# Kernel tuning notes

Measured on AMD Instinct MI355X. Metric: run time of the kernel, lower is better.

Reference implementation:

```python
import jax, jax.numpy as jnp
import numpy as np

N_ATOMS = 3
HIDDEN = 256
N_PAIRS = N_ATOMS * (N_ATOMS - 1) // 2  # 3
BATCH = 500000


def setup_inputs() -> dict:
    key = jax.random.key(0)
    ks = jax.random.split(key, 8)
    s1 = 1.0 / np.sqrt(N_PAIRS)
    s2 = 1.0 / np.sqrt(HIDDEN)
    return {
        "x": jax.random.normal(ks[0], (BATCH, N_ATOMS * 3), dtype=jnp.float32),
        "W1": jax.random.normal(ks[1], (N_PAIRS, HIDDEN), dtype=jnp.float32) * s1,
        "b1": jnp.zeros((HIDDEN,), dtype=jnp.float32),
        "W2": jax.random.normal(ks[2], (HIDDEN, HIDDEN), dtype=jnp.float32) * s2,
        "b2": jnp.zeros((HIDDEN,), dtype=jnp.float32),
        "W3": jax.random.normal(ks[3], (HIDDEN, 3), dtype=jnp.float32) * s2,
        "b3": jnp.zeros((3,), dtype=jnp.float32),
    }


def reference(x, W1, b1, W2, b2, W3, b3):
    # --- pairwise bond lengths (vectorized over batch) ---
    pts = x.reshape(-1, N_ATOMS, 3)                       # [B, n_atoms, 3]
    iu, ju = np.triu_indices(N_ATOMS, 1)                  # static index arrays
    diff = pts[:, iu, :] - pts[:, ju, :]                  # [B, n_pairs, 3]
    r = jnp.sqrt(jnp.sum(diff * diff, axis=-1))           # [B, n_pairs]
    # --- MLP: Dense->relu->Dense->relu->Dense (sizes=[256,256,3]) ---
    h = jax.nn.relu(r @ W1 + b1)                          # [B, 256]
    h = jax.nn.relu(h @ W2 + b2)                          # [B, 256]
    w = h @ W3 + b3                                       # [B, 3] -> (w00, w11, w01)
    # --- analytic eigenvalues of symmetric 2x2 [[w00,w01],[w01,w11]] ---
    # eigh returns ascending order: mean -/+ radius
    m = 0.5 * (w[:, 0] + w[:, 1])
    d = 0.5 * (w[:, 0] - w[:, 1])
    rad = jnp.sqrt(d * d + w[:, 2] * w[:, 2])
    return jnp.stack([m - rad, m + rad], axis=-1)         # [B, 2]
```

## Files before the change

kernel.cpp:

```cpp
#include <hip/hip_runtime.h>
#include <hip/hip_bf16.h>
#include <stdint.h>

typedef __attribute__((ext_vector_type(8))) short short8;
typedef __attribute__((ext_vector_type(4))) float f32x4;

#define NCHUNK 15625
#define NBLK 256
#define NTHR 512
#define NWAVE_TOT (NBLK * 8)

#define FRAG_OFF   0
#define W1_OFF     131072
#define B2_OFF     135168
#define SCR_OFF    136192
#define LDS_TOTAL  152576

__device__ __forceinline__ uint32_t cvtpk(float lo, float hi) {
    uint32_t r;
    asm("v_cvt_pk_bf16_f32 %0, %1, %2" : "=v"(r) : "v"(lo), "v"(hi));
    return r;
}

__device__ __forceinline__ int sig2(int mp) {
    int t = mp >> 4, gm = (mp >> 2) & 3, r = mp & 3;
    return ((t >> 1) << 5) + (gm << 3) + ((t & 1) << 2) + r;
}

__global__ __launch_bounds__(NTHR, 2) void fused_kernel(
    const float* __restrict__ x,  const float* __restrict__ W1,
    const float* __restrict__ b1, const float* __restrict__ W2,
    const float* __restrict__ b2, const float* __restrict__ W3,
    const float* __restrict__ b3, float* __restrict__ out)
{
    extern __shared__ char smem[];
    uint4*  frag4 = (uint4*)(smem + FRAG_OFF);
    float4* w1lds = (float4*)(smem + W1_OFF);
    float4* b2lds = (float4*)(smem + B2_OFF);
    float*  scrf  = (float*)(smem + SCR_OFF);
    uint4*  scr4  = (uint4*)(smem + SCR_OFF);

    const int tid  = threadIdx.x;
    const int lane = tid & 63;
    const int g    = lane >> 4;
    const int lr   = lane & 15;

    if (tid < 256)
        w1lds[tid] = make_float4(W1[tid], W1[256 + tid], W1[512 + tid], b1[tid]);
    else if (tid < 320)
        b2lds[tid - 256] = ((const float4*)b2)[tid - 256];

    const uint4* gw2 = (const uint4*)W2;
    for (int p = 0; p < 16; ++p) {
        __syncthreads();
        scr4[tid]       = gw2[p * 1024 + tid];
        scr4[tid + 512] = gw2[p * 1024 + 512 + tid];
        __syncthreads();
        int t   = tid >> 5;
        int l   = (tid & 31) + ((p & 1) << 5);
        int c16 = l & 15;
        int s   = p >> 1;
        int c   = sig2(t * 16 + c16);
        int rowbase = ((l >> 4) & 1) * 8;
        float f[8];
#pragma unroll
        for (int j = 0; j < 8; ++j) f[j] = scrf[(rowbase + j) * 256 + c];
        uint4 wv;
        wv.x = cvtpk(f[0], f[1]); wv.y = cvtpk(f[2], f[3]);
        wv.z = cvtpk(f[4], f[5]); wv.w = cvtpk(f[6], f[7]);
        frag4[(s * 16 + t) * 64 + l] = wv;
    }
    __syncthreads();

    short8 w3f[8];
#pragma unroll
    for (int s2 = 0; s2 < 8; ++s2) {
        float f3[8];
#pragma unroll
        for (int j = 0; j < 8; ++j) {
            int kk = s2 * 32 + g * 8 + j;
            f3[j] = (lr < 3) ? W3[kk * 3 + lr] : 0.0f;
        }
        union { short8 s8; uint32_t u[4]; } pw;
        pw.u[0] = cvtpk(f3[0], f3[1]); pw.u[1] = cvtpk(f3[2], f3[3]);
        pw.u[2] = cvtpk(f3[4], f3[5]); pw.u[3] = cvtpk(f3[6], f3[7]);
        w3f[s2] = pw.s8;
    }
    const float b30 = b3[0], b31 = b3[1], b32 = b3[2];

    const short8* afr = (const short8*)(smem + FRAG_OFF);
    const int gwave = blockIdx.x * 8 + (tid >> 6);

    for (int chunk = gwave; chunk < NCHUNK; chunk += NWAVE_TOT) {
        const int row0 = chunk * 32;

        float q0[2], q1[2], q2[2];
#pragma unroll
        for (int nt = 0; nt < 2; ++nt) {
            const float* xp = x + (size_t)(row0 + nt * 16 + lr) * 9;
            float a0 = xp[0], a1 = xp[1], a2 = xp[2], a3 = xp[3], a4 = xp[4];
            float a5 = xp[5], a6 = xp[6], a7 = xp[7], a8 = xp[8];
            float d0 = a0 - a3, d1 = a1 - a4, d2 = a2 - a5;
            float e0 = a0 - a6, e1 = a1 - a7, e2 = a2 - a8;
            float f0 = a3 - a6, f1 = a4 - a7, f2 = a5 - a8;
            q0[nt] = sqrtf(fmaf(d0, d0, fmaf(d1, d1, d2 * d2)));
            q1[nt] = sqrtf(fmaf(e0, e0, fmaf(e1, e1, e2 * e2)));
            q2[nt] = sqrtf(fmaf(f0, f0, fmaf(f1, f1, f2 * f2)));
        }

        f32x4 acc[16][2];
#pragma unroll
        for (int t = 0; t < 16; ++t) {
            int bc4 = (((t >> 1) << 5) + (g << 3) + ((t & 1) << 2)) >> 2;
            float4 bv = b2lds[bc4];
            f32x4 bi; bi[0] = bv.x; bi[1] = bv.y; bi[2] = bv.z; bi[3] = bv.w;
            acc[t][0] = bi; acc[t][1] = bi;
        }

#pragma unroll 1
        for (int s = 0; s < 8; ++s) {
            float4 wv[8];
#pragma unroll
            for (int j = 0; j < 8; ++j) wv[j] = w1lds[s * 32 + g * 8 + j];
            short8 hb[2];
#pragma unroll
            for (int nt = 0; nt < 2; ++nt) {
                union { short8 s8; uint32_t u[4]; } pk;
#pragma unroll
                for (int jj = 0; jj < 4; ++jj) {
                    float4 wa = wv[2 * jj], wb = wv[2 * jj + 1];
                    float ha = fmaf(q0[nt], wa.x, fmaf(q1[nt], wa.y, fmaf(q2[nt], wa.z, wa.w)));
                    float hc = fmaf(q0[nt], wb.x, fmaf(q1[nt], wb.y, fmaf(q2[nt], wb.z, wb.w)));
                    pk.u[jj] = cvtpk(fmaxf(ha, 0.f), fmaxf(hc, 0.f));
                }
                hb[nt] = pk.s8;
            }
#pragma unroll
            for (int t = 0; t < 16; ++t) {
                short8 av = afr[(s * 16 + t) * 64 + lane];
                acc[t][0] = __builtin_amdgcn_mfma_f32_16x16x32_bf16(av, hb[0], acc[t][0], 0, 0, 0);
                acc[t][1] = __builtin_amdgcn_mfma_f32_16x16x32_bf16(av, hb[1], acc[t][1], 0, 0, 0);
            }
        }

#pragma unroll
        for (int nt = 0; nt < 2; ++nt) {
            f32x4 D = {0.f, 0.f, 0.f, 0.f};
#pragma unroll
            for (int s2 = 0; s2 < 8; ++s2) {
                union { short8 s8; uint32_t u[4]; } pb;
                pb.u[0] = cvtpk(fmaxf(acc[2 * s2][nt][0], 0.f), fmaxf(acc[2 * s2][nt][1], 0.f));
                pb.u[1] = cvtpk(fmaxf(acc[2 * s2][nt][2], 0.f), fmaxf(acc[2 * s2][nt][3], 0.f));
                pb.u[2] = cvtpk(fmaxf(acc[2 * s2 + 1][nt][0], 0.f), fmaxf(acc[2 * s2 + 1][nt][1], 0.f));
                pb.u[3] = cvtpk(fmaxf(acc[2 * s2 + 1][nt][2], 0.f), fmaxf(acc[2 * s2 + 1][nt][3], 0.f));
                D = __builtin_amdgcn_mfma_f32_16x16x32_bf16(w3f[s2], pb.s8, D, 0, 0, 0);
            }
            if (g == 0) {
                float w0 = D[0] + b30, w1v = D[1] + b31, wc = D[2] + b32;
                float mm = 0.5f * (w0 + w1v), dd = 0.5f * (w0 - w1v);
                float rad = sqrtf(fmaf(dd, dd, wc * wc));
                int row = row0 + nt * 16 + lr;
                *(float2*)(out + (size_t)row * 2) = make_float2(mm - rad, mm + rad);
            }
        }
    }
}

extern "C" void kernel_launch(void* const* d_in, const int* in_sizes, int n_in,
                              void* d_out, int out_size, void* d_ws, size_t ws_size,
                              hipStream_t stream) {
    const float* x  = (const float*)d_in[0];
    const float* W1 = (const float*)d_in[1];
    const float* b1 = (const float*)d_in[2];
    const float* W2 = (const float*)d_in[3];
    const float* b2 = (const float*)d_in[4];
    const float* W3 = (const float*)d_in[5];
    const float* b3 = (const float*)d_in[6];
    float* out = (float*)d_out;

    (void)d_ws; (void)ws_size;

    (void)hipFuncSetAttribute((const void*)fused_kernel,
                              hipFuncAttributeMaxDynamicSharedMemorySize, LDS_TOTAL);

    fused_kernel<<<NBLK, NTHR, LDS_TOTAL, stream>>>(x, W1, b1, W2, b2, W3, b3, out);
}
```

Baseline: 159.1 us.

## Switch to 32x32x16 MFMA, compute layer 1 and bias via MFMA, prefetch x

Replaces the 16x16x32 MFMA tiling with 32x32x16 bf16 MFMAs, so each wave handles one 32-row chunk with 8 accumulator tiles. Layer 1 (bond lengths times W1 plus b1) and the b2 bias initialisation now run as MFMAs against padded fragments in LDS, replacing the VALU FMA loops. W2 fragments are repacked with a swizzled column layout to match. The next chunk's x rows are prefetched into registers to hide global load latency. This reduces VALU work and load stalls, at the cost of extra wasted MFMA work on zero-padded operands and higher register pressure.

```diff
diff --git a/kernel.cpp b/kernel.cpp
--- a/kernel.cpp
+++ b/kernel.cpp
@@ -2,29 +2,27 @@
 #include <hip/hip_bf16.h>
 #include <stdint.h>
 
-typedef __attribute__((ext_vector_type(8))) short short8;
-typedef __attribute__((ext_vector_type(4))) float f32x4;
+typedef __attribute__((ext_vector_type(8)))  short short8;
+typedef __attribute__((ext_vector_type(16))) float f32x16;
 
 #define NCHUNK 15625
 #define NBLK 256
 #define NTHR 512
 #define NWAVE_TOT (NBLK * 8)
 
-#define FRAG_OFF   0
-#define W1_OFF     131072
-#define B2_OFF     135168
-#define SCR_OFF    136192
-#define LDS_TOTAL  152576
+#define SW(v) ((((v) & ~12u)) | (((v) & 4u) << 1) | (((v) & 8u) >> 1))
+
+#define A2_OFF   0
+#define A1_OFF   131072
+#define Z_OFF    135168
+#define A3_OFF   135184
+#define SCR_OFF  136720
+#define LDS_TOTAL 153104
 
 __device__ __forceinline__ uint32_t cvtpk(float lo, float hi) {
     uint32_t r;
     asm("v_cvt_pk_bf16_f32 %0, %1, %2" : "=v"(r) : "v"(lo), "v"(hi));
     return r;
-}
-
-__device__ __forceinline__ int sig2(int mp) {
-    int t = mp >> 4, gm = (mp >> 2) & 3, r = mp & 3;
-    return ((t >> 1) << 5) + (gm << 3) + ((t & 1) << 2) + r;
 }
 
 __global__ __launch_bounds__(NTHR, 2) void fused_kernel(
@@ -34,135 +32,153 @@
     const float* __restrict__ b3, float* __restrict__ out)
 {
     extern __shared__ char smem[];
-    uint4*  frag4 = (uint4*)(smem + FRAG_OFF);
-    float4* w1lds = (float4*)(smem + W1_OFF);
-    float4* b2lds = (float4*)(smem + B2_OFF);
-    float*  scrf  = (float*)(smem + SCR_OFF);
-    uint4*  scr4  = (uint4*)(smem + SCR_OFF);
-
-    const int tid  = threadIdx.x;
-    const int lane = tid & 63;
-    const int g    = lane >> 4;
-    const int lr   = lane & 15;
-
-    if (tid < 256)
-        w1lds[tid] = make_float4(W1[tid], W1[256 + tid], W1[512 + tid], b1[tid]);
-    else if (tid < 320)
-        b2lds[tid - 256] = ((const float4*)b2)[tid - 256];
-
+    uint4* frag4 = (uint4*)(smem + A2_OFF);
+    float* scrf  = (float*)(smem + SCR_OFF);
+    uint4* scr4  = (uint4*)(smem + SCR_OFF);
+
+    const int tid = threadIdx.x;
+    const int l   = tid & 63;
+    const int hi  = l >> 5;
+    const int c   = l & 31;
+
+    {
+        int fr = tid >> 6, l2 = tid & 63;
+        if (l2 < 32) {
+            int row = fr * 32 + l2;
+            uint4 v;
+            v.x = cvtpk(W1[row], W1[256 + row]);
+            v.y = cvtpk(W1[512 + row], b1[row]);
+            v.z = 0; v.w = 0;
+            ((uint4*)(smem + A1_OFF))[fr * 32 + l2] = v;
+        }
+        if (tid == 511) ((uint4*)(smem + Z_OFF))[0] = make_uint4(0, 0, 0, 0);
+        if (tid < 96) {
+            int fr3 = tid / 6, rem = tid % 6, hi2 = rem / 3, c2 = rem % 3;
+            int kb = 16 * fr3 + 8 * hi2;
+            uint4 v;
+            v.x = cvtpk(W3[(kb + 0) * 3 + c2], W3[(kb + 1) * 3 + c2]);
+            v.y = cvtpk(W3[(kb + 2) * 3 + c2], W3[(kb + 3) * 3 + c2]);
+            v.z = cvtpk(W3[(kb + 4) * 3 + c2], W3[(kb + 5) * 3 + c2]);
+            v.w = cvtpk(W3[(kb + 6) * 3 + c2], W3[(kb + 7) * 3 + c2]);
+            ((uint4*)(smem + A3_OFF))[fr3 * 6 + rem] = v;
+        }
+    }
     const uint4* gw2 = (const uint4*)W2;
-    for (int p = 0; p < 16; ++p) {
+    for (int kt = 0; kt < 16; ++kt) {
         __syncthreads();
-        scr4[tid]       = gw2[p * 1024 + tid];
-        scr4[tid + 512] = gw2[p * 1024 + 512 + tid];
+        scr4[tid]       = gw2[kt * 1024 + tid];
+        scr4[tid + 512] = gw2[kt * 1024 + 512 + tid];
         __syncthreads();
-        int t   = tid >> 5;
-        int l   = (tid & 31) + ((p & 1) << 5);
-        int c16 = l & 15;
-        int s   = p >> 1;
-        int c   = sig2(t * 16 + c16);
-        int rowbase = ((l >> 4) & 1) * 8;
+        int mt = tid >> 6, l2 = tid & 63, hi2 = l2 >> 5, c2 = l2 & 31;
+        int col = 32 * mt + (int)SW((unsigned)c2);
         float f[8];
 #pragma unroll
-        for (int j = 0; j < 8; ++j) f[j] = scrf[(rowbase + j) * 256 + c];
-        uint4 wv;
-        wv.x = cvtpk(f[0], f[1]); wv.y = cvtpk(f[2], f[3]);
-        wv.z = cvtpk(f[4], f[5]); wv.w = cvtpk(f[6], f[7]);
-        frag4[(s * 16 + t) * 64 + l] = wv;
+        for (int j = 0; j < 8; ++j) {
+            int lrow = 8 * (j >> 2) + 4 * hi2 + (j & 3);
+            f[j] = scrf[lrow * 256 + col];
+        }
+        uint4 v;
+        v.x = cvtpk(f[0], f[1]); v.y = cvtpk(f[2], f[3]);
+        v.z = cvtpk(f[4], f[5]); v.w = cvtpk(f[6], f[7]);
+        frag4[(kt * 8 + mt) * 64 + l2] = v;
     }
     __syncthreads();
 
-    short8 w3f[8];
-#pragma unroll
-    for (int s2 = 0; s2 < 8; ++s2) {
-        float f3[8];
-#pragma unroll
-        for (int j = 0; j < 8; ++j) {
-            int kk = s2 * 32 + g * 8 + j;
-            f3[j] = (lr < 3) ? W3[kk * 3 + lr] : 0.0f;
-        }
-        union { short8 s8; uint32_t u[4]; } pw;
-        pw.u[0] = cvtpk(f3[0], f3[1]); pw.u[1] = cvtpk(f3[2], f3[3]);
-        pw.u[2] = cvtpk(f3[4], f3[5]); pw.u[3] = cvtpk(f3[6], f3[7]);
-        w3f[s2] = pw.s8;
-    }
+    const f32x16 Z = {0,0,0,0,0,0,0,0,0,0,0,0,0,0,0,0};
+    uint32_t b2pk[8];
+#pragma unroll
+    for (int mt = 0; mt < 8; ++mt)
+        b2pk[mt] = hi ? 0u : cvtpk(b2[32 * mt + (int)SW((unsigned)c)], 0.0f);
+    union { short8 s8; uint32_t u[4]; } bB;
+    bB.u[0] = hi ? 0u : 0x3F80u; bB.u[1] = 0; bB.u[2] = 0; bB.u[3] = 0;
+    const short8 biasB = bB.s8;
     const float b30 = b3[0], b31 = b3[1], b32 = b3[2];
 
-    const short8* afr = (const short8*)(smem + FRAG_OFF);
+    const int a1step = hi ? 0 : 512;
+    const int a1base = hi ? Z_OFF : (A1_OFF + c * 16);
+    const int a3step = (c < 3) ? 96 : 0;
+    const int a3base = (c < 3) ? (A3_OFF + (hi * 3 + c) * 16) : Z_OFF;
+
     const int gwave = blockIdx.x * 8 + (tid >> 6);
 
+    float xb[9], xn[9];
+    {
+        const float* xp = x + (size_t)(gwave * 32 + c) * 9;
+#pragma unroll
+        for (int j = 0; j < 9; ++j) xb[j] = xp[j];
+    }
+
     for (int chunk = gwave; chunk < NCHUNK; chunk += NWAVE_TOT) {
-        const int row0 = chunk * 32;
-
-        float q0[2], q1[2], q2[2];
-#pragma unroll
-        for (int nt = 0; nt < 2; ++nt) {
-            const float* xp = x + (size_t)(row0 + nt * 16 + lr) * 9;
-            float a0 = xp[0], a1 = xp[1], a2 = xp[2], a3 = xp[3], a4 = xp[4];
-            float a5 = xp[5], a6 = xp[6], a7 = xp[7], a8 = xp[8];
-            float d0 = a0 - a3, d1 = a1 - a4, d2 = a2 - a5;
-            float e0 = a0 - a6, e1 = a1 - a7, e2 = a2 - a8;
-            float f0 = a3 - a6, f1 = a4 - a7, f2 = a5 - a8;
-            q0[nt] = sqrtf(fmaf(d0, d0, fmaf(d1, d1, d2 * d2)));
-            q1[nt] = sqrtf(fmaf(e0, e0, fmaf(e1, e1, e2 * e2)));
-            q2[nt] = sqrtf(fmaf(f0, f0, fmaf(f1, f1, f2 * f2)));
-        }
-
-        f32x4 acc[16][2];
-#pragma unroll
-        for (int t = 0; t < 16; ++t) {
-            int bc4 = (((t >> 1) << 5) + (g << 3) + ((t & 1) << 2)) >> 2;
-            float4 bv = b2lds[bc4];
-            f32x4 bi; bi[0] = bv.x; bi[1] = bv.y; bi[2] = bv.z; bi[3] = bv.w;
-            acc[t][0] = bi; acc[t][1] = bi;
-        }
-
-#pragma unroll 1
-        for (int s = 0; s < 8; ++s) {
-            float4 wv[8];
-#pragma unroll
-            for (int j = 0; j < 8; ++j) wv[j] = w1lds[s * 32 + g * 8 + j];
-            short8 hb[2];
-#pragma unroll
-            for (int nt = 0; nt < 2; ++nt) {
+        {
+            int nxt = chunk + NWAVE_TOT;
+            const float* xpn = x + (size_t)(((nxt < NCHUNK) ? nxt : chunk) * 32 + c) * 9;
+#pragma unroll
+            for (int j = 0; j < 9; ++j) xn[j] = xpn[j];
+        }
+        float d0 = xb[0] - xb[3], d1 = xb[1] - xb[4], d2 = xb[2] - xb[5];
+        float e0 = xb[0] - xb[6], e1 = xb[1] - xb[7], e2 = xb[2] - xb[8];
+        float f0 = xb[3] - xb[6], f1 = xb[4] - xb[7], f2 = xb[5] - xb[8];
+        float q0 = sqrtf(fmaf(d0, d0, fmaf(d1, d1, d2 * d2)));
+        float q1 = sqrtf(fmaf(e0, e0, fmaf(e1, e1, e2 * e2)));
+        float q2 = sqrtf(fmaf(f0, f0, fmaf(f1, f1, f2 * f2)));
+
+        union { short8 s8; uint32_t u[4]; } qf;
+        qf.u[0] = hi ? 0u : cvtpk(q0, q1);
+        qf.u[1] = hi ? 0u : cvtpk(q2, 1.0f);
+        qf.u[2] = 0; qf.u[3] = 0;
+        const short8 qfrag = qf.s8;
+
+        f32x16 acc[8];
+#pragma unroll
+        for (int mt = 0; mt < 8; ++mt) {
+            union { short8 s8; uint32_t u[4]; } bA;
+            bA.u[0] = b2pk[mt]; bA.u[1] = 0; bA.u[2] = 0; bA.u[3] = 0;
+            acc[mt] = __builtin_amdgcn_mfma_f32_32x32x16_bf16(bA.s8, biasB, Z, 0, 0, 0);
+        }
+
+#pragma unroll
+        for (int tau = 0; tau < 8; ++tau) {
+            short8 a1 = *(const short8*)(smem + a1base + tau * a1step);
+            f32x16 d1v = __builtin_amdgcn_mfma_f32_32x32x16_bf16(a1, qfrag, Z, 0, 0, 0);
+#pragma unroll
+            for (int p = 0; p < 2; ++p) {
+                const int kt = 2 * tau + p;
                 union { short8 s8; uint32_t u[4]; } pk;
 #pragma unroll
-                for (int jj = 0; jj < 4; ++jj) {
-                    float4 wa = wv[2 * jj], wb = wv[2 * jj + 1];
-                    float ha = fmaf(q0[nt], wa.x, fmaf(q1[nt], wa.y, fmaf(q2[nt], wa.z, wa.w)));
-                    float hc = fmaf(q0[nt], wb.x, fmaf(q1[nt], wb.y, fmaf(q2[nt], wb.z, wb.w)));
-                    pk.u[jj] = cvtpk(fmaxf(ha, 0.f), fmaxf(hc, 0.f));
+                for (int w = 0; w < 4; ++w)
+                    pk.u[w] = cvtpk(fmaxf(d1v[8 * p + 2 * w], 0.0f),
+                                    fmaxf(d1v[8 * p + 2 * w + 1], 0.0f));
+                const short8 bfr = pk.s8;
+#pragma unroll
+                for (int mt = 0; mt < 8; ++mt) {
+                    short8 a2 = *(const short8*)(smem + (size_t)(kt * 8 + mt) * 1024 + l * 16);
+                    acc[mt] = __builtin_amdgcn_mfma_f32_32x32x16_bf16(a2, bfr, acc[mt], 0, 0, 0);
                 }
-                hb[nt] = pk.s8;
             }
-#pragma unroll
-            for (int t = 0; t < 16; ++t) {
-                short8 av = afr[(s * 16 + t) * 64 + lane];
-                acc[t][0] = __builtin_amdgcn_mfma_f32_16x16x32_bf16(av, hb[0], acc[t][0], 0, 0, 0);
-                acc[t][1] = __builtin_amdgcn_mfma_f32_16x16x32_bf16(av, hb[1], acc[t][1], 0, 0, 0);
-            }
-        }
-
-#pragma unroll
-        for (int nt = 0; nt < 2; ++nt) {
-            f32x4 D = {0.f, 0.f, 0.f, 0.f};
-#pragma unroll
-            for (int s2 = 0; s2 < 8; ++s2) {
-                union { short8 s8; uint32_t u[4]; } pb;
-                pb.u[0] = cvtpk(fmaxf(acc[2 * s2][nt][0], 0.f), fmaxf(acc[2 * s2][nt][1], 0.f));
-                pb.u[1] = cvtpk(fmaxf(acc[2 * s2][nt][2], 0.f), fmaxf(acc[2 * s2][nt][3], 0.f));
-                pb.u[2] = cvtpk(fmaxf(acc[2 * s2 + 1][nt][0], 0.f), fmaxf(acc[2 * s2 + 1][nt][1], 0.f));
-                pb.u[3] = cvtpk(fmaxf(acc[2 * s2 + 1][nt][2], 0.f), fmaxf(acc[2 * s2 + 1][nt][3], 0.f));
-                D = __builtin_amdgcn_mfma_f32_16x16x32_bf16(w3f[s2], pb.s8, D, 0, 0, 0);
-            }
-            if (g == 0) {
-                float w0 = D[0] + b30, w1v = D[1] + b31, wc = D[2] + b32;
-                float mm = 0.5f * (w0 + w1v), dd = 0.5f * (w0 - w1v);
-                float rad = sqrtf(fmaf(dd, dd, wc * wc));
-                int row = row0 + nt * 16 + lr;
-                *(float2*)(out + (size_t)row * 2) = make_float2(mm - rad, mm + rad);
-            }
-        }
+        }
+
+        f32x16 d3 = Z;
+#pragma unroll
+        for (int kt3 = 0; kt3 < 16; ++kt3) {
+            const int mt = kt3 >> 1, p = kt3 & 1;
+            union { short8 s8; uint32_t u[4]; } pk;
+#pragma unroll
+            for (int w = 0; w < 4; ++w)
+                pk.u[w] = cvtpk(fmaxf(acc[mt][8 * p + 2 * w], 0.0f),
+                                fmaxf(acc[mt][8 * p + 2 * w + 1], 0.0f));
+            short8 a3 = *(const short8*)(smem + a3base + kt3 * a3step);
+            d3 = __builtin_amdgcn_mfma_f32_32x32x16_bf16(a3, pk.s8, d3, 0, 0, 0);
+        }
+
+        if (hi == 0) {
+            float w0 = d3[0] + b30, w1v = d3[1] + b31, wc = d3[2] + b32;
+            float mm = 0.5f * (w0 + w1v), dd = 0.5f * (w0 - w1v);
+            float rad = sqrtf(fmaf(dd, dd, wc * wc));
+            *(float2*)(out + (size_t)(chunk * 32 + c) * 2) = make_float2(mm - rad, mm + rad);
+        }
+
+#pragma unroll
+        for (int j = 0; j < 9; ++j) xb[j] = xn[j];
     }
 }
 
```

Result: faster. 145.0 us (-8.8%).
